# Kernel tuning notes

Measured on AMD Instinct MI355X. Metric: run time of the kernel, lower is better.

Reference implementation:

```python
import jax, jax.numpy as jnp
import numpy as np

NUM_EMBED = 1024
HEAD_SIZE = 64
B, T = 4, 4096

def setup_inputs() -> dict:
    key = jax.random.key(0)
    kx, kq, kk, kv = jax.random.split(key, 4)
    scale = NUM_EMBED ** -0.5
    return {
        "x": jax.random.normal(kx, (B, T, NUM_EMBED), dtype=jnp.float32),
        "Wq": jax.random.normal(kq, (NUM_EMBED, HEAD_SIZE), dtype=jnp.float32) * scale,
        "Wk": jax.random.normal(kk, (NUM_EMBED, HEAD_SIZE), dtype=jnp.float32) * scale,
        "Wv": jax.random.normal(kv, (NUM_EMBED, HEAD_SIZE), dtype=jnp.float32) * scale,
    }

def reference(x, Wq, Wk, Wv):
    # x: [B,T,C]; Wq/Wk/Wv: [C,H]
    q = jnp.einsum('btc,ch->bth', x, Wq)
    k = jnp.einsum('btc,ch->bth', x, Wk)
    v = jnp.einsum('btc,ch->bth', x, Wv)
    Tq = x.shape[1]
    att = jnp.einsum('bth,bsh->bts', q, k) * (k.shape[-1] ** -0.5)  # [B,T,T]
    causal = jnp.tril(jnp.ones((Tq, Tq), dtype=bool))
    att = jnp.where(causal, att, -jnp.inf)
    att = jax.nn.softmax(att, axis=-1)
    # dropout p=0 (eval mode): identity
    out = jnp.einsum('bts,bsh->bth', att, v)  # [B,T,H]
    return out
```

## Files before the change

kernel.cpp:

```cpp
#include <hip/hip_runtime.h>

#define B_ 4
#define T_ 4096
#define C_ 1024
#define H_ 64

typedef _Float16 half8  __attribute__((ext_vector_type(8)));
typedef _Float16 half4_ __attribute__((ext_vector_type(4)));
typedef float    floatx4 __attribute__((ext_vector_type(4)));

#define MFMA16(a, b, c) __builtin_amdgcn_mfma_f32_16x16x32_f16(a, b, c, 0, 0, 0)

__global__ __launch_bounds__(256) void pack_w_kn(
    const float* __restrict__ Wq, const float* __restrict__ Wk,
    const float* __restrict__ Wv, _Float16* __restrict__ Wt2)
{
    const int idx  = blockIdx.x * 256 + threadIdx.x;
    const int mt   = idx >> 14;
    const int j    = (idx >> 10) & 15;
    const int f    = (idx >> 9) & 1;
    const int lane = (idx >> 3) & 63;
    const int jj   = idx & 7;
    const int q = lane >> 4, c = lane & 15;
    const int k  = j * 64 + f * 32 + q * 8 + jj;
    const int hp = mt * 16 + c;
    const float* W = (hp < 64) ? Wq : (hp < 128) ? Wk : Wv;
    Wt2[idx] = (_Float16)W[k * H_ + (hp & 63)];
}

__global__ __launch_bounds__(512) void qkv_kn(
    const float* __restrict__ x, const _Float16* __restrict__ Wt2,
    _Float16* __restrict__ Qh, _Float16* __restrict__ Kpk,
    _Float16* __restrict__ Vpk)
{
    __shared__ _Float16 xs[2][32][72];
    const int tid  = threadIdx.x;
    const int lane = tid & 63, w = tid >> 6;
    const int q    = lane >> 4, c = lane & 15;
    const int nt   = w & 1;
    const int mg   = w >> 1;
    const int row0 = blockIdx.x * 32;

    const int srow = tid >> 4, scol = (tid & 15) * 4;
    const float* xg = x + (size_t)(row0 + srow) * C_ + scol;

    floatx4 acc[3];
    #pragma unroll
    for (int i = 0; i < 3; ++i) acc[i] = floatx4{0.f, 0.f, 0.f, 0.f};

    float4 g = *(const float4*)xg;

    for (int j = 0; j < 16; ++j) {
        half4_ hv;
        hv[0] = (_Float16)g.x; hv[1] = (_Float16)g.y;
        hv[2] = (_Float16)g.z; hv[3] = (_Float16)g.w;
        *(half4_*)(&xs[j & 1][srow][scol]) = hv;
        __syncthreads();
        if (j < 15) g = *(const float4*)(xg + (j + 1) * 64);

        const _Float16* xrow = &xs[j & 1][nt * 16 + c][q * 8];
        const half8 b0 = *(const half8*)xrow;
        const half8 b1 = *(const half8*)(xrow + 32);

        half8 a[6];
        #pragma unroll
        for (int i = 0; i < 3; ++i) {
            const size_t fb = ((size_t)((mg * 3 + i) * 16 + j) * 2) * 512 + lane * 8;
            a[i * 2]     = *(const half8*)(Wt2 + fb);
            a[i * 2 + 1] = *(const half8*)(Wt2 + fb + 512);
        }
        #pragma unroll
        for (int i = 0; i < 3; ++i) {
            acc[i] = MFMA16(a[i * 2],     b0, acc[i]);
            acc[i] = MFMA16(a[i * 2 + 1], b1, acc[i]);
        }
    }

    const int row = row0 + nt * 16 + c;
    const int b = row >> 12, t4 = row & (T_ - 1);
    const int kt = t4 >> 6;
    const size_t tbase = ((size_t)b * 64 + kt) * 4096;
    const int mtk = (t4 >> 4) & 3;
    const int kk  = t4 & 63;

    #pragma unroll
    for (int i = 0; i < 3; ++i) {
        const int gi = mg * 3 + i;
        if (gi < 4) {
            half4_ v;
            #pragma unroll
            for (int r = 0; r < 4; ++r) v[r] = (_Float16)acc[i][r];
            *(half4_*)(Qh + (size_t)row * H_ + gi * 16 + q * 4) = v;
        } else if (gi < 8) {
            half4_ v;
            #pragma unroll
            for (int r = 0; r < 4; ++r) v[r] = (_Float16)acc[i][r];
            const int e  = gi - 4;
            const int f  = e >> 1;
            const int qa = (e * 2 + (q >> 1)) & 3;
            *(half4_*)(Kpk + tbase + ((size_t)(mtk * 2 + f) * 64 + qa * 16 + c) * 8
                       + (q & 1) * 4) = v;
        } else {
            const int mtv = gi - 8;
            const int qa = (kk >> 3) & 3, fv = kk >> 5, jv = kk & 7;
            #pragma unroll
            for (int r = 0; r < 4; ++r) {
                const int cv = q * 4 + r;
                Vpk[tbase + ((size_t)(mtv * 2 + fv) * 64 + qa * 16 + cv) * 8 + jv]
                    = (_Float16)acc[i][r];
            }
        }
    }
}

__global__ __launch_bounds__(512, 4) void attn_kn(
    const _Float16* __restrict__ Qh, const _Float16* __restrict__ Kpk,
    const _Float16* __restrict__ Vpk, float* __restrict__ out)
{
    __shared__ __align__(16) char smem[36864];
    const int lane = threadIdx.x & 63;
    const int w    = threadIdx.x >> 6;
    const int q    = lane >> 4, c = lane & 15;

    const int bid  = blockIdx.x;
    const int xcd  = bid & 7;
    const int slot = bid >> 3;
    const int b    = xcd >> 1;
    const int tr   = (slot << 1) | (xcd & 1);
    const int t    = 255 - tr;

    const int row0 = t * 16;
    const int grow = b * T_ + row0;
    const int nk   = (t >> 2) + 1;

    _Float16* Pw = (_Float16*)smem + w * 2304;

    half8 bq0 = *(const half8*)(Qh + (size_t)(grow + c) * H_ + q * 8);
    half8 bq1 = *(const half8*)(Qh + (size_t)(grow + c) * H_ + 32 + q * 8);
    const _Float16 qs = (_Float16)0.18033688f;
    bq0 *= qs; bq1 *= qs;

    floatx4 o[4];
    #pragma unroll
    for (int i = 0; i < 4; ++i) o[i] = floatx4{0.f, 0.f, 0.f, 0.f};
    float m = -3.0e38f, l = 0.f;

    for (int kt = w; kt < nk; kt += 8) {
        const int kb = kt * 64;
        const _Float16* Kt = Kpk + ((size_t)b * 64 + kt) * 4096;
        const _Float16* Vt = Vpk + ((size_t)b * 64 + kt) * 4096;
        half8 a0[4], a1[4];

        #pragma unroll
        for (int mt = 0; mt < 4; ++mt) {
            a0[mt] = *(const half8*)(Kt + ((size_t)(mt * 2)     * 64 + lane) * 8);
            a1[mt] = *(const half8*)(Kt + ((size_t)(mt * 2 + 1) * 64 + lane) * 8);
        }
        floatx4 s[4];
        #pragma unroll
        for (int mt = 0; mt < 4; ++mt) {
            floatx4 z = floatx4{0.f, 0.f, 0.f, 0.f};
            z = MFMA16(a0[mt], bq0, z);
            s[mt] = MFMA16(a1[mt], bq1, z);
        }
        #pragma unroll
        for (int mt = 0; mt < 4; ++mt) {
            a0[mt] = *(const half8*)(Vt + ((size_t)(mt * 2)     * 64 + lane) * 8);
            a1[mt] = *(const half8*)(Vt + ((size_t)(mt * 2 + 1) * 64 + lane) * 8);
        }

        if (kt == nk - 1) {
            #pragma unroll
            for (int mt = 0; mt < 4; ++mt)
                #pragma unroll
                for (int r = 0; r < 4; ++r)
                    if (kb + mt * 16 + q * 4 + r > row0 + c) s[mt][r] = -3.0e38f;
        }

        float mx = s[0][0];
        #pragma unroll
        for (int mt = 0; mt < 4; ++mt)
            #pragma unroll
            for (int r = 0; r < 4; ++r) mx = fmaxf(mx, s[mt][r]);
        mx = fmaxf(mx, __shfl_xor(mx, 16, 64));
        mx = fmaxf(mx, __shfl_xor(mx, 32, 64));
        const float mn    = fmaxf(m, mx);
        const float alpha = exp2f(m - mn);
        float p[4][4];
        float sl = 0.f;
        #pragma unroll
        for (int mt = 0; mt < 4; ++mt)
            #pragma unroll
            for (int r = 0; r < 4; ++r) {
                p[mt][r] = exp2f(s[mt][r] - mn);
                sl += p[mt][r];
            }
        sl += __shfl_xor(sl, 16, 64);
        sl += __shfl_xor(sl, 32, 64);
        l = l * alpha + sl;
        m = mn;
        #pragma unroll
        for (int mt = 0; mt < 4; ++mt)
            #pragma unroll
            for (int r = 0; r < 4; ++r) o[mt][r] *= alpha;

        _Float16* pl = Pw + ((kt >> 3) & 1) * 1152 + c * 72;
        #pragma unroll
        for (int mt = 0; mt < 4; ++mt) {
            half4_ ph;
            #pragma unroll
            for (int r = 0; r < 4; ++r) ph[r] = (_Float16)p[mt][r];
            *(half4_*)(pl + mt * 16 + q * 4) = ph;
        }
        const half8 bp0 = *(const half8*)(pl + q * 8);
        const half8 bp1 = *(const half8*)(pl + 32 + q * 8);

        #pragma unroll
        for (int mt = 0; mt < 4; ++mt) {
            o[mt] = MFMA16(a0[mt], bp0, o[mt]);
            o[mt] = MFMA16(a1[mt], bp1, o[mt]);
        }
    }

    __syncthreads();
    float* Ol = (float*)smem;
    float* Ml = (float*)(smem + 34816);
    float* Ll = (float*)(smem + 35328);
    if (q == 0) Ml[w * 16 + c] = m;
    __syncthreads();
    float M = Ml[c];
    #pragma unroll
    for (int w2 = 1; w2 < 8; ++w2) M = fmaxf(M, Ml[w2 * 16 + c]);
    const float alpha = exp2f(m - M);
    if (q == 0) Ll[w * 16 + c] = l * alpha;
    #pragma unroll
    for (int mt = 0; mt < 4; ++mt)
        #pragma unroll
        for (int r = 0; r < 4; ++r)
            Ol[w * 1088 + (mt * 16 + q * 4 + r) * 17 + c] = o[mt][r] * alpha;
    __syncthreads();

    float L = 0.f;
    #pragma unroll
    for (int w2 = 0; w2 < 8; ++w2) L += Ll[w2 * 16 + c];
    const float inv = 1.f / L;
    const int h0 = w * 8 + q * 2;
    float ox = 0.f, oy = 0.f;
    #pragma unroll
    for (int w2 = 0; w2 < 8; ++w2) {
        ox += Ol[w2 * 1088 + h0 * 17 + c];
        oy += Ol[w2 * 1088 + (h0 + 1) * 17 + c];
    }
    float2 st; st.x = ox * inv; st.y = oy * inv;
    *(float2*)(out + (size_t)(grow + c) * H_ + h0) = st;
}

extern "C" void kernel_launch(void* const* d_in, const int* in_sizes, int n_in,
                              void* d_out, int out_size, void* d_ws, size_t ws_size,
                              hipStream_t stream) {
    const float* x  = (const float*)d_in[0];
    const float* Wq = (const float*)d_in[1];
    const float* Wk = (const float*)d_in[2];
    const float* Wv = (const float*)d_in[3];
    float* out = (float*)d_out;

    _Float16* ws = (_Float16*)d_ws;
    _Float16* Wt2 = ws;
    _Float16* Qh  = ws + 196608;
    _Float16* Kpk = Qh + 1048576;
    _Float16* Vpk = Kpk + 1048576;

    hipLaunchKernelGGL(pack_w_kn, dim3(768), dim3(256), 0, stream, Wq, Wk, Wv, Wt2);
    hipLaunchKernelGGL(qkv_kn, dim3((B_ * T_) / 32), dim3(512), 0, stream,
                       x, Wt2, Qh, Kpk, Vpk);
    hipLaunchKernelGGL(attn_kn, dim3(1024), dim3(512), 0, stream,
                       Qh, Kpk, Vpk, out);
}
```

Before: 140.2 us.

## Process 32 query rows per attention block to reuse K/V tiles

```diff
diff --git a/kernel.cpp b/kernel.cpp
--- a/kernel.cpp
+++ b/kernel.cpp
@@ -117,7 +117,7 @@
     const _Float16* __restrict__ Qh, const _Float16* __restrict__ Kpk,
     const _Float16* __restrict__ Vpk, float* __restrict__ out)
 {
-    __shared__ __align__(16) char smem[36864];
+    __shared__ __align__(16) char smem[73728];
     const int lane = threadIdx.x & 63;
     const int w    = threadIdx.x >> 6;
     const int q    = lane >> 4, c = lane & 15;
@@ -126,24 +126,30 @@
     const int xcd  = bid & 7;
     const int slot = bid >> 3;
     const int b    = xcd >> 1;
-    const int tr   = (slot << 1) | (xcd & 1);
-    const int t    = 255 - tr;
-
-    const int row0 = t * 16;
+    const int t32  = 127 - ((slot << 1) | (xcd & 1));
+
+    const int row0 = t32 * 32;
     const int grow = b * T_ + row0;
-    const int nk   = (t >> 2) + 1;
-
-    _Float16* Pw = (_Float16*)smem + w * 2304;
-
-    half8 bq0 = *(const half8*)(Qh + (size_t)(grow + c) * H_ + q * 8);
-    half8 bq1 = *(const half8*)(Qh + (size_t)(grow + c) * H_ + 32 + q * 8);
+    const int nk   = (t32 >> 1) + 1;
+
+    _Float16* Pw = (_Float16*)smem + w * 4608;
+
     const _Float16 qs = (_Float16)0.18033688f;
-    bq0 *= qs; bq1 *= qs;
-
-    floatx4 o[4];
-    #pragma unroll
-    for (int i = 0; i < 4; ++i) o[i] = floatx4{0.f, 0.f, 0.f, 0.f};
-    float m = -3.0e38f, l = 0.f;
+    half8 bq0[2], bq1[2];
+    #pragma unroll
+    for (int g = 0; g < 2; ++g) {
+        const _Float16* qb = Qh + (size_t)(grow + g * 16 + c) * H_;
+        bq0[g] = *(const half8*)(qb + q * 8);
+        bq1[g] = *(const half8*)(qb + 32 + q * 8);
+        bq0[g] *= qs; bq1[g] *= qs;
+    }
+
+    floatx4 o[4][2];
+    #pragma unroll
+    for (int i = 0; i < 4; ++i)
+        #pragma unroll
+        for (int g = 0; g < 2; ++g) o[i][g] = floatx4{0.f, 0.f, 0.f, 0.f};
+    float m[2] = {-3.0e38f, -3.0e38f}, l[2] = {0.f, 0.f};
 
     for (int kt = w; kt < nk; kt += 8) {
         const int kb = kt * 64;
@@ -156,13 +162,15 @@
             a0[mt] = *(const half8*)(Kt + ((size_t)(mt * 2)     * 64 + lane) * 8);
             a1[mt] = *(const half8*)(Kt + ((size_t)(mt * 2 + 1) * 64 + lane) * 8);
         }
-        floatx4 s[4];
-        #pragma unroll
-        for (int mt = 0; mt < 4; ++mt) {
-            floatx4 z = floatx4{0.f, 0.f, 0.f, 0.f};
-            z = MFMA16(a0[mt], bq0, z);
-            s[mt] = MFMA16(a1[mt], bq1, z);
-        }
+        floatx4 s[4][2];
+        #pragma unroll
+        for (int mt = 0; mt < 4; ++mt)
+            #pragma unroll
+            for (int g = 0; g < 2; ++g) {
+                floatx4 z = floatx4{0.f, 0.f, 0.f, 0.f};
+                z = MFMA16(a0[mt], bq0[g], z);
+                s[mt][g] = MFMA16(a1[mt], bq1[g], z);
+            }
         #pragma unroll
         for (int mt = 0; mt < 4; ++mt) {
             a0[mt] = *(const half8*)(Vt + ((size_t)(mt * 2)     * 64 + lane) * 8);
@@ -173,86 +181,100 @@
             #pragma unroll
             for (int mt = 0; mt < 4; ++mt)
                 #pragma unroll
-                for (int r = 0; r < 4; ++r)
-                    if (kb + mt * 16 + q * 4 + r > row0 + c) s[mt][r] = -3.0e38f;
-        }
-
-        float mx = s[0][0];
+                for (int g = 0; g < 2; ++g)
+                    #pragma unroll
+                    for (int r = 0; r < 4; ++r)
+                        if (kb + mt * 16 + q * 4 + r > row0 + g * 16 + c)
+                            s[mt][g][r] = -3.0e38f;
+        }
+
+        _Float16* Pb = Pw + ((kt >> 3) & 1) * 2304;
+        #pragma unroll
+        for (int g = 0; g < 2; ++g) {
+            float mx = s[0][g][0];
+            #pragma unroll
+            for (int mt = 0; mt < 4; ++mt)
+                #pragma unroll
+                for (int r = 0; r < 4; ++r) mx = fmaxf(mx, s[mt][g][r]);
+            mx = fmaxf(mx, __shfl_xor(mx, 16, 64));
+            mx = fmaxf(mx, __shfl_xor(mx, 32, 64));
+            const float mn    = fmaxf(m[g], mx);
+            const float alpha = exp2f(m[g] - mn);
+            _Float16* pl = Pb + g * 1152 + c * 72;
+            float sl = 0.f;
+            #pragma unroll
+            for (int mt = 0; mt < 4; ++mt) {
+                half4_ ph;
+                #pragma unroll
+                for (int r = 0; r < 4; ++r) {
+                    const float e = exp2f(s[mt][g][r] - mn);
+                    sl += e;
+                    ph[r] = (_Float16)e;
+                }
+                *(half4_*)(pl + mt * 16 + q * 4) = ph;
+            }
+            sl += __shfl_xor(sl, 16, 64);
+            sl += __shfl_xor(sl, 32, 64);
+            l[g] = l[g] * alpha + sl;
+            m[g] = mn;
+            #pragma unroll
+            for (int mt = 0; mt < 4; ++mt) o[mt][g] *= alpha;
+        }
+
+        half8 bp0[2], bp1[2];
+        #pragma unroll
+        for (int g = 0; g < 2; ++g) {
+            const _Float16* pl = Pb + g * 1152 + c * 72;
+            bp0[g] = *(const half8*)(pl + q * 8);
+            bp1[g] = *(const half8*)(pl + 32 + q * 8);
+        }
         #pragma unroll
         for (int mt = 0; mt < 4; ++mt)
             #pragma unroll
-            for (int r = 0; r < 4; ++r) mx = fmaxf(mx, s[mt][r]);
-        mx = fmaxf(mx, __shfl_xor(mx, 16, 64));
-        mx = fmaxf(mx, __shfl_xor(mx, 32, 64));
-        const float mn    = fmaxf(m, mx);
-        const float alpha = exp2f(m - mn);
-        float p[4][4];
-        float sl = 0.f;
-        #pragma unroll
-        for (int mt = 0; mt < 4; ++mt)
-            #pragma unroll
-            for (int r = 0; r < 4; ++r) {
-                p[mt][r] = exp2f(s[mt][r] - mn);
-                sl += p[mt][r];
+            for (int g = 0; g < 2; ++g) {
+                o[mt][g] = MFMA16(a0[mt], bp0[g], o[mt][g]);
+                o[mt][g] = MFMA16(a1[mt], bp1[g], o[mt][g]);
             }
-        sl += __shfl_xor(sl, 16, 64);
-        sl += __shfl_xor(sl, 32, 64);
-        l = l * alpha + sl;
-        m = mn;
-        #pragma unroll
-        for (int mt = 0; mt < 4; ++mt)
-            #pragma unroll
-            for (int r = 0; r < 4; ++r) o[mt][r] *= alpha;
-
-        _Float16* pl = Pw + ((kt >> 3) & 1) * 1152 + c * 72;
-        #pragma unroll
-        for (int mt = 0; mt < 4; ++mt) {
-            half4_ ph;
-            #pragma unroll
-            for (int r = 0; r < 4; ++r) ph[r] = (_Float16)p[mt][r];
-            *(half4_*)(pl + mt * 16 + q * 4) = ph;
-        }
-        const half8 bp0 = *(const half8*)(pl + q * 8);
-        const half8 bp1 = *(const half8*)(pl + 32 + q * 8);
-
-        #pragma unroll
-        for (int mt = 0; mt < 4; ++mt) {
-            o[mt] = MFMA16(a0[mt], bp0, o[mt]);
-            o[mt] = MFMA16(a1[mt], bp1, o[mt]);
-        }
     }
 
     __syncthreads();
     float* Ol = (float*)smem;
-    float* Ml = (float*)(smem + 34816);
-    float* Ll = (float*)(smem + 35328);
-    if (q == 0) Ml[w * 16 + c] = m;
+    float* Ml = (float*)(smem + 69632);
+    float* Ll = (float*)(smem + 70656);
+    if (q == 0) { Ml[w * 32 + c] = m[0]; Ml[w * 32 + 16 + c] = m[1]; }
     __syncthreads();
-    float M = Ml[c];
-    #pragma unroll
-    for (int w2 = 1; w2 < 8; ++w2) M = fmaxf(M, Ml[w2 * 16 + c]);
-    const float alpha = exp2f(m - M);
-    if (q == 0) Ll[w * 16 + c] = l * alpha;
+    float M0 = Ml[c], M1 = Ml[16 + c];
+    #pragma unroll
+    for (int w2 = 1; w2 < 8; ++w2) {
+        M0 = fmaxf(M0, Ml[w2 * 32 + c]);
+        M1 = fmaxf(M1, Ml[w2 * 32 + 16 + c]);
+    }
+    const float alpha0 = exp2f(m[0] - M0);
+    const float alpha1 = exp2f(m[1] - M1);
+    if (q == 0) { Ll[w * 32 + c] = l[0] * alpha0; Ll[w * 32 + 16 + c] = l[1] * alpha1; }
     #pragma unroll
     for (int mt = 0; mt < 4; ++mt)
         #pragma unroll
+        for (int r = 0; r < 4; ++r) {
+            Ol[w * 2176 + (mt * 16 + q * 4 + r) * 17 + c]        = o[mt][0][r] * alpha0;
+            Ol[w * 2176 + (64 + mt * 16 + q * 4 + r) * 17 + c]   = o[mt][1][r] * alpha1;
+        }
+    __syncthreads();
+
+    const int g  = w & 1;
+    const int h0 = (w >> 1) * 16 + q * 4;
+    float L = 0.f;
+    #pragma unroll
+    for (int w2 = 0; w2 < 8; ++w2) L += Ll[w2 * 32 + g * 16 + c];
+    const float inv = 1.f / L;
+    floatx4 st = floatx4{0.f, 0.f, 0.f, 0.f};
+    #pragma unroll
+    for (int w2 = 0; w2 < 8; ++w2)
+        #pragma unroll
         for (int r = 0; r < 4; ++r)
-            Ol[w * 1088 + (mt * 16 + q * 4 + r) * 17 + c] = o[mt][r] * alpha;
-    __syncthreads();
-
-    float L = 0.f;
-    #pragma unroll
-    for (int w2 = 0; w2 < 8; ++w2) L += Ll[w2 * 16 + c];
-    const float inv = 1.f / L;
-    const int h0 = w * 8 + q * 2;
-    float ox = 0.f, oy = 0.f;
-    #pragma unroll
-    for (int w2 = 0; w2 < 8; ++w2) {
-        ox += Ol[w2 * 1088 + h0 * 17 + c];
-        oy += Ol[w2 * 1088 + (h0 + 1) * 17 + c];
-    }
-    float2 st; st.x = ox * inv; st.y = oy * inv;
-    *(float2*)(out + (size_t)(grow + c) * H_ + h0) = st;
+            st[r] += Ol[w2 * 2176 + (g * 64 + h0 + r) * 17 + c];
+    st *= inv;
+    *(floatx4*)(out + (size_t)(grow + g * 16 + c) * H_ + h0) = st;
 }
 
 extern "C" void kernel_launch(void* const* d_in, const int* in_sizes, int n_in,
@@ -273,6 +295,6 @@
     hipLaunchKernelGGL(pack_w_kn, dim3(768), dim3(256), 0, stream, Wq, Wk, Wv, Wt2);
     hipLaunchKernelGGL(qkv_kn, dim3((B_ * T_) / 32), dim3(512), 0, stream,
                        x, Wt2, Qh, Kpk, Vpk);
-    hipLaunchKernelGGL(attn_kn, dim3(1024), dim3(512), 0, stream,
+    hipLaunchKernelGGL(attn_kn, dim3(512), dim3(512), 0, stream,
                        Qh, Kpk, Vpk, out);
 }
```

Result: slower. 171.1 us (+22.0%).

## Prefetch next K tile, keep P in registers, lazily rescale softmax

Applied to the files above, without the earlier changes.

```diff
diff --git a/kernel.cpp b/kernel.cpp
--- a/kernel.cpp
+++ b/kernel.cpp
@@ -9,7 +9,10 @@
 typedef _Float16 half4_ __attribute__((ext_vector_type(4)));
 typedef float    floatx4 __attribute__((ext_vector_type(4)));
 
-#define MFMA16(a, b, c) __builtin_amdgcn_mfma_f32_16x16x32_f16(a, b, c, 0, 0, 0)
+#define MFMA16(a, b, c)  __builtin_amdgcn_mfma_f32_16x16x32_f16(a, b, c, 0, 0, 0)
+#define MFMA16K(a, b, c) __builtin_amdgcn_mfma_f32_16x16x16f16(a, b, c, 0, 0, 0)
+#define LO4(v) __builtin_shufflevector(v, v, 0, 1, 2, 3)
+#define HI4(v) __builtin_shufflevector(v, v, 4, 5, 6, 7)
 
 __global__ __launch_bounds__(256) void pack_w_kn(
     const float* __restrict__ Wq, const float* __restrict__ Wk,
@@ -102,12 +105,15 @@
                        + (q & 1) * 4) = v;
         } else {
             const int mtv = gi - 8;
-            const int qa = (kk >> 3) & 3, fv = kk >> 5, jv = kk & 7;
+            const int qa2 = (kk >> 2) & 3;
+            const int h4  = (kk >> 4) & 1;
+            const int f2  = kk >> 5;
+            const int i2  = kk & 3;
             #pragma unroll
             for (int r = 0; r < 4; ++r) {
                 const int cv = q * 4 + r;
-                Vpk[tbase + ((size_t)(mtv * 2 + fv) * 64 + qa * 16 + cv) * 8 + jv]
-                    = (_Float16)acc[i][r];
+                Vpk[tbase + ((size_t)(mtv * 2 + f2) * 64 + qa2 * 16 + cv) * 8
+                    + h4 * 4 + i2] = (_Float16)acc[i][r];
             }
         }
     }
@@ -126,14 +132,10 @@
     const int xcd  = bid & 7;
     const int slot = bid >> 3;
     const int b    = xcd >> 1;
-    const int tr   = (slot << 1) | (xcd & 1);
-    const int t    = 255 - tr;
-
+    const int t    = 255 - ((slot << 1) | (xcd & 1));
     const int row0 = t * 16;
     const int grow = b * T_ + row0;
     const int nk   = (t >> 2) + 1;
-
-    _Float16* Pw = (_Float16*)smem + w * 2304;
 
     half8 bq0 = *(const half8*)(Qh + (size_t)(grow + c) * H_ + q * 8);
     half8 bq1 = *(const half8*)(Qh + (size_t)(grow + c) * H_ + 32 + q * 8);
@@ -145,28 +147,47 @@
     for (int i = 0; i < 4; ++i) o[i] = floatx4{0.f, 0.f, 0.f, 0.f};
     float m = -3.0e38f, l = 0.f;
 
+    const _Float16* Kb = Kpk + (size_t)b * 262144;
+    const _Float16* Vb = Vpk + (size_t)b * 262144;
+
+    half8 k0[4], k1[4], v0[4], v1[4];
+    {
+        const _Float16* Kt = Kb + (size_t)w * 4096;
+        #pragma unroll
+        for (int mt = 0; mt < 4; ++mt) {
+            k0[mt] = *(const half8*)(Kt + ((mt * 2)     * 64 + lane) * 8);
+            k1[mt] = *(const half8*)(Kt + ((mt * 2 + 1) * 64 + lane) * 8);
+        }
+    }
+
+    #pragma unroll 1
     for (int kt = w; kt < nk; kt += 8) {
         const int kb = kt * 64;
-        const _Float16* Kt = Kpk + ((size_t)b * 64 + kt) * 4096;
-        const _Float16* Vt = Vpk + ((size_t)b * 64 + kt) * 4096;
-        half8 a0[4], a1[4];
-
-        #pragma unroll
-        for (int mt = 0; mt < 4; ++mt) {
-            a0[mt] = *(const half8*)(Kt + ((size_t)(mt * 2)     * 64 + lane) * 8);
-            a1[mt] = *(const half8*)(Kt + ((size_t)(mt * 2 + 1) * 64 + lane) * 8);
-        }
+
         floatx4 s[4];
+        __builtin_amdgcn_s_setprio(1);
         #pragma unroll
         for (int mt = 0; mt < 4; ++mt) {
             floatx4 z = floatx4{0.f, 0.f, 0.f, 0.f};
-            z = MFMA16(a0[mt], bq0, z);
-            s[mt] = MFMA16(a1[mt], bq1, z);
-        }
-        #pragma unroll
-        for (int mt = 0; mt < 4; ++mt) {
-            a0[mt] = *(const half8*)(Vt + ((size_t)(mt * 2)     * 64 + lane) * 8);
-            a1[mt] = *(const half8*)(Vt + ((size_t)(mt * 2 + 1) * 64 + lane) * 8);
+            z = MFMA16(k0[mt], bq0, z);
+            s[mt] = MFMA16(k1[mt], bq1, z);
+        }
+        __builtin_amdgcn_s_setprio(0);
+
+        const _Float16* Vt = Vb + (size_t)kt * 4096;
+        #pragma unroll
+        for (int mt = 0; mt < 4; ++mt) {
+            v0[mt] = *(const half8*)(Vt + ((mt * 2)     * 64 + lane) * 8);
+            v1[mt] = *(const half8*)(Vt + ((mt * 2 + 1) * 64 + lane) * 8);
+        }
+        {
+            const int ktn = (kt + 8 < nk) ? (kt + 8) : kt;
+            const _Float16* Kt = Kb + (size_t)ktn * 4096;
+            #pragma unroll
+            for (int mt = 0; mt < 4; ++mt) {
+                k0[mt] = *(const half8*)(Kt + ((mt * 2)     * 64 + lane) * 8);
+                k1[mt] = *(const half8*)(Kt + ((mt * 2 + 1) * 64 + lane) * 8);
+            }
         }
 
         if (kt == nk - 1) {
@@ -184,45 +205,39 @@
             for (int r = 0; r < 4; ++r) mx = fmaxf(mx, s[mt][r]);
         mx = fmaxf(mx, __shfl_xor(mx, 16, 64));
         mx = fmaxf(mx, __shfl_xor(mx, 32, 64));
-        const float mn    = fmaxf(m, mx);
-        const float alpha = exp2f(m - mn);
-        float p[4][4];
+        if (!__all(mx <= m + 8.f)) {
+            const float mn    = fmaxf(m, mx);
+            const float alpha = exp2f(m - mn);
+            l *= alpha;
+            #pragma unroll
+            for (int mt = 0; mt < 4; ++mt) o[mt] *= alpha;
+            m = mn;
+        }
+        half4_ ph[4];
         float sl = 0.f;
         #pragma unroll
         for (int mt = 0; mt < 4; ++mt)
             #pragma unroll
             for (int r = 0; r < 4; ++r) {
-                p[mt][r] = exp2f(s[mt][r] - mn);
-                sl += p[mt][r];
+                const float ev = exp2f(s[mt][r] - m);
+                sl += ev;
+                ph[mt][r] = (_Float16)ev;
             }
         sl += __shfl_xor(sl, 16, 64);
         sl += __shfl_xor(sl, 32, 64);
-        l = l * alpha + sl;
-        m = mn;
-        #pragma unroll
-        for (int mt = 0; mt < 4; ++mt)
-            #pragma unroll
-            for (int r = 0; r < 4; ++r) o[mt][r] *= alpha;
-
-        _Float16* pl = Pw + ((kt >> 3) & 1) * 1152 + c * 72;
-        #pragma unroll
-        for (int mt = 0; mt < 4; ++mt) {
-            half4_ ph;
-            #pragma unroll
-            for (int r = 0; r < 4; ++r) ph[r] = (_Float16)p[mt][r];
-            *(half4_*)(pl + mt * 16 + q * 4) = ph;
-        }
-        const half8 bp0 = *(const half8*)(pl + q * 8);
-        const half8 bp1 = *(const half8*)(pl + 32 + q * 8);
-
-        #pragma unroll
-        for (int mt = 0; mt < 4; ++mt) {
-            o[mt] = MFMA16(a0[mt], bp0, o[mt]);
-            o[mt] = MFMA16(a1[mt], bp1, o[mt]);
-        }
-    }
-
-    __syncthreads();
+        l += sl;
+
+        __builtin_amdgcn_s_setprio(1);
+        #pragma unroll
+        for (int mt = 0; mt < 4; ++mt) {
+            o[mt] = MFMA16K(LO4(v0[mt]), ph[0], o[mt]);
+            o[mt] = MFMA16K(HI4(v0[mt]), ph[1], o[mt]);
+            o[mt] = MFMA16K(LO4(v1[mt]), ph[2], o[mt]);
+            o[mt] = MFMA16K(HI4(v1[mt]), ph[3], o[mt]);
+        }
+        __builtin_amdgcn_s_setprio(0);
+    }
+
     float* Ol = (float*)smem;
     float* Ml = (float*)(smem + 34816);
     float* Ll = (float*)(smem + 35328);
```

Result: no change. 138.0 us (-1.6%).
